# Optimization experiments

Hardware: AMD Instinct MI355X
Metric: run time of the kernel (lower is better)

## Reference

```python
import jax, jax.numpy as jnp
import numpy as np
import math

DIM = 1024
N_HEADS = 16
HEAD_DIM = DIM // N_HEADS


def setup_inputs() -> dict:
    key = jax.random.key(0)
    kx, kk, kq, kv = jax.random.split(key, 4)
    x = jax.random.normal(kx, (4, 2048, DIM), dtype=jnp.float32)
    # torch.rand -> uniform [0,1)
    wk = jax.random.uniform(kk, (N_HEADS, DIM, HEAD_DIM), dtype=jnp.float32)
    wq = jax.random.uniform(kq, (N_HEADS, DIM, HEAD_DIM), dtype=jnp.float32)
    wv = jax.random.uniform(kv, (N_HEADS, DIM, HEAD_DIM), dtype=jnp.float32)
    return {"x": x, "wk": wk, "wq": wq, "wv": wv}


def reference(x, wk, wq, wv):
    # x: [b, l, d]; w*: [n, d, e]
    k = jnp.einsum('bld,nde->bnle', x, wk)
    q = jnp.einsum('bld,nde->bnle', x, wq)
    v = jnp.einsum('bld,nde->bnle', x, wv)
    head_dim = k.shape[-1]
    scores = jnp.einsum('bnle,bnme->bnlm', q, k) / math.sqrt(head_dim)
    s = jax.nn.softmax(scores, axis=-1)
    r = jnp.einsum('bnlm,bnme->blne', s, v)  # [b, l, n, e]
    b, l, n, e = r.shape
    return r.reshape(b, l, n * e)
```

## Files before the change

kernel.cpp:

```cpp
#include <hip/hip_runtime.h>
#include <math.h>

#define DIMX   1024
#define NHEADS 16
#define HD     64
#define BATCH  4
#define SEQ    2048
#define NM     (BATCH * NHEADS * SEQ * HD)

typedef unsigned short ushort_t;
typedef __attribute__((ext_vector_type(8))) short bf16x8;
typedef __attribute__((ext_vector_type(4))) short bf16x4;
typedef __attribute__((ext_vector_type(4))) float f32x4;

#define MFMA16(a, b, c) __builtin_amdgcn_mfma_f32_16x16x32_bf16(a, b, c, 0, 0, 0)

#if __has_builtin(__builtin_amdgcn_mfma_f32_16x16x16bf16_1k)
#define MFMA_PV(a, b, c) __builtin_amdgcn_mfma_f32_16x16x16bf16_1k(a, b, c, 0, 0, 0)
#else
static __device__ __forceinline__ f32x4 mfma_pv_asm(bf16x4 a, bf16x4 b, f32x4 c) {
    asm("v_mfma_f32_16x16x16_bf16 %0, %1, %2, %0" : "+v"(c) : "v"(a), "v"(b));
    return c;
}
#define MFMA_PV(a, b, c) mfma_pv_asm(a, b, c)
#endif

__device__ __forceinline__ ushort_t f2bf(float x) {
    unsigned u = __float_as_uint(x);
    u += 0x7fffu + ((u >> 16) & 1u);
    return (ushort_t)(u >> 16);
}
__device__ __forceinline__ float bf2f(ushort_t h) {
    return __uint_as_float(((unsigned)h) << 16);
}

__device__ __forceinline__ unsigned pack_bf16_trunc(float lo, float hi) {
#if __has_builtin(__builtin_amdgcn_perm)
    return __builtin_amdgcn_perm(__float_as_uint(hi), __float_as_uint(lo), 0x07060302u);
#else
    return (__float_as_uint(lo) >> 16) | (__float_as_uint(hi) & 0xFFFF0000u);
#endif
}
__device__ __forceinline__ float trunc_bf(float x) {
    return __uint_as_float(__float_as_uint(x) & 0xFFFF0000u);
}

__device__ __forceinline__ float fast_exp2(float x) {
#if __has_builtin(__builtin_amdgcn_exp2f)
    return __builtin_amdgcn_exp2f(x);
#else
    return exp2f(x);
#endif
}

#define GLOAD_LDS16(g, l) \
    __builtin_amdgcn_global_load_lds((const __attribute__((address_space(1))) unsigned int*)(g), \
                                     (__attribute__((address_space(3))) unsigned int*)(l), 16, 0, 0)

__global__ __launch_bounds__(256) void convert_x(
    const float* __restrict__ x, ushort_t* __restrict__ Xh, ushort_t* __restrict__ Xl)
{
    int i = blockIdx.x * 256 + threadIdx.x;
    #pragma unroll
    for (int t = 0; t < 4; t++) {
        int idx = t * 524288 + i;
        f32x4 v = ((const f32x4*)x)[idx];
        ushort4 hi, lo;
        hi.x = f2bf(v[0]); lo.x = f2bf(v[0] - bf2f(hi.x));
        hi.y = f2bf(v[1]); lo.y = f2bf(v[1] - bf2f(hi.y));
        hi.z = f2bf(v[2]); lo.z = f2bf(v[2] - bf2f(hi.z));
        hi.w = f2bf(v[3]); lo.w = f2bf(v[3] - bf2f(hi.w));
        ((ushort4*)Xh)[idx] = hi;
        ((ushort4*)Xl)[idx] = lo;
    }
}

__global__ __launch_bounds__(256) void convert_w(
    const float* __restrict__ wk, const float* __restrict__ wq, const float* __restrict__ wv,
    ushort_t* __restrict__ Bqh, ushort_t* __restrict__ Bql, ushort_t* __restrict__ Bvh)
{
    __shared__ float Ts[64][65];
    const int bid = blockIdx.x;
    const int mat = bid >> 8;
    const int rem = bid & 255;
    const int n  = rem >> 4;
    const int dt = rem & 15;
    const float* w = (mat == 0) ? wq : (mat == 1) ? wk : wv;
    const int tid = threadIdx.x;

    #pragma unroll
    for (int t = 0; t < 16; t++) {
        int i = tid + t * 256;
        int r = i >> 6, e = i & 63;
        Ts[r][e] = w[((size_t)n * 1024 + dt * 64 + r) * 64 + e];
    }
    __syncthreads();
    #pragma unroll
    for (int t = 0; t < 16; t++) {
        int i = tid + t * 256;
        int e = i >> 6, r = i & 63;
        float v = Ts[r][e];
        ushort_t hi = f2bf(v);
        size_t o = (size_t)(n * 64 + e) * 1024 + dt * 64 + r;
        if (mat < 2) {
            Bqh[(size_t)mat * 1048576 + o] = hi;
            Bql[(size_t)mat * 1048576 + o] = f2bf(v - bf2f(hi));
        } else {
            Bvh[o] = hi;
        }
    }
}

__global__ __launch_bounds__(256) void proj_qk(
    const ushort_t* __restrict__ Xh, const ushort_t* __restrict__ Xl,
    const ushort_t* __restrict__ Bh, const ushort_t* __restrict__ Bl,
    float* __restrict__ Qf, ushort_t* __restrict__ Khi, ushort_t* __restrict__ Klo)
{
    __shared__ __align__(16) ushort_t Ah[128 * 64];
    __shared__ __align__(16) ushort_t Al[128 * 64];
    __shared__ __align__(16) ushort_t Bhs[128 * 64];
    __shared__ __align__(16) ushort_t Bls[128 * 64];

    const int mt = blockIdx.x, nt = blockIdx.y;
    const int tid = threadIdx.x;
    const int w = tid >> 6, lane = tid & 63, col = lane & 15, quad = lane >> 4;
    const int wm = w & 1, wn = w >> 1;

    f32x4 acc[4][4] = {};

    for (int kc = 0; kc < 1024; kc += 64) {
        __syncthreads();
        #pragma unroll
        for (int i = 0; i < 4; i++) {
            int s = (w * 4 + i) * 64 + lane;
            int r = s >> 3, j = s & 7, g = j ^ (r & 7);
            size_t aoff = (size_t)(mt * 128 + r) * 1024 + kc + g * 8;
            size_t boff = (size_t)(nt * 128 + r) * 1024 + kc + g * 8;
            GLOAD_LDS16(Xh + aoff, Ah  + (size_t)(w * 4 + i) * 512);
            GLOAD_LDS16(Xl + aoff, Al  + (size_t)(w * 4 + i) * 512);
            GLOAD_LDS16(Bh + boff, Bhs + (size_t)(w * 4 + i) * 512);
            GLOAD_LDS16(Bl + boff, Bls + (size_t)(w * 4 + i) * 512);
        }
        __syncthreads();
        #pragma unroll
        for (int kk = 0; kk < 2; kk++) {
            bf16x8 a_h[4], a_l[4], b_h[4], b_l[4];
            const int gi = kk * 4 + quad;
            #pragma unroll
            for (int t = 0; t < 4; t++) {
                int rA = wm * 64 + t * 16 + col;
                int jA = gi ^ (rA & 7);
                a_h[t] = *(const bf16x8*)&Ah[(rA * 8 + jA) * 8];
                a_l[t] = *(const bf16x8*)&Al[(rA * 8 + jA) * 8];
                int rB = wn * 64 + t * 16 + col;
                int jB = gi ^ (rB & 7);
                b_h[t] = *(const bf16x8*)&Bhs[(rB * 8 + jB) * 8];
                b_l[t] = *(const bf16x8*)&Bls[(rB * 8 + jB) * 8];
            }
            #pragma unroll
            for (int t = 0; t < 4; t++)
                #pragma unroll
                for (int u = 0; u < 4; u++) {
                    acc[t][u] = MFMA16(a_h[t], b_h[u], acc[t][u]);
                    acc[t][u] = MFMA16(a_l[t], b_h[u], acc[t][u]);
                    acc[t][u] = MFMA16(a_h[t], b_l[u], acc[t][u]);
                }
        }
    }

    const bool isQ = (nt < 8);
    #pragma unroll
    for (int t = 0; t < 4; t++) {
        #pragma unroll
        for (int u = 0; u < 4; u++) {
            int np = nt * 128 + wn * 64 + u * 16 + col;
            int head = (np >> 6) & 15, e = np & 63;
            #pragma unroll
            for (int rr = 0; rr < 4; rr++) {
                int mm = mt * 128 + wm * 64 + t * 16 + quad * 4 + rr;
                int bi = mm >> 11, l = mm & 2047;
                size_t base = (((size_t)bi * NHEADS + head) * SEQ + l) * HD + e;
                float v = acc[t][u][rr];
                if (isQ) {
                    Qf[base] = v;
                } else {
                    ushort_t hi = f2bf(v);
                    Khi[base] = hi;
                    Klo[base] = f2bf(v - bf2f(hi));
                }
            }
        }
    }
}

__global__ __launch_bounds__(256) void proj_v(
    const ushort_t* __restrict__ Wvh, const ushort_t* __restrict__ Xh,
    ushort_t* __restrict__ Vt)
{
    __shared__ __align__(16) ushort_t Ah[128 * 64];
    __shared__ __align__(16) ushort_t Bhs[128 * 64];

    const int mt = blockIdx.x, nt = blockIdx.y;
    const int tid = threadIdx.x;
    const int w = tid >> 6, lane = tid & 63, col = lane & 15, quad = lane >> 4;
    const int wm = w & 1, wn = w >> 1;

    f32x4 acc[4][4] = {};

    for (int kc = 0; kc < 1024; kc += 64) {
        __syncthreads();
        #pragma unroll
        for (int i = 0; i < 4; i++) {
            int s = (w * 4 + i) * 64 + lane;
            int r = s >> 3, j = s & 7, g = j ^ (r & 7);
            size_t aoff = (size_t)(mt * 128 + r) * 1024 + kc + g * 8;
            size_t boff = (size_t)(nt * 128 + r) * 1024 + kc + g * 8;
            GLOAD_LDS16(Wvh + aoff, Ah  + (size_t)(w * 4 + i) * 512);
            GLOAD_LDS16(Xh  + boff, Bhs + (size_t)(w * 4 + i) * 512);
        }
        __syncthreads();
        #pragma unroll
        for (int kk = 0; kk < 2; kk++) {
            bf16x8 a_h[4], b_h[4];
            const int gi = kk * 4 + quad;
            #pragma unroll
            for (int t = 0; t < 4; t++) {
                int rA = wm * 64 + t * 16 + col;
                a_h[t] = *(const bf16x8*)&Ah[(rA * 8 + (gi ^ (rA & 7))) * 8];
                int rB = wn * 64 + t * 16 + col;
                b_h[t] = *(const bf16x8*)&Bhs[(rB * 8 + (gi ^ (rB & 7))) * 8];
            }
            #pragma unroll
            for (int t = 0; t < 4; t++)
                #pragma unroll
                for (int u = 0; u < 4; u++)
                    acc[t][u] = MFMA16(a_h[t], b_h[u], acc[t][u]);
        }
    }

    #pragma unroll
    for (int t = 0; t < 4; t++) {
        #pragma unroll
        for (int rr = 0; rr < 4; rr++) {
            int ep = mt * 128 + wm * 64 + t * 16 + quad * 4 + rr;
            int head = ep >> 6, e = ep & 63;
            #pragma unroll
            for (int u = 0; u < 4; u++) {
                int lg = nt * 128 + wn * 64 + u * 16 + col;
                int bi = lg >> 11, l = lg & 2047;
                Vt[(((size_t)bi * NHEADS + head) * HD + e) * SEQ + l] = f2bf(acc[t][u][rr]);
            }
        }
    }
}

__global__ __launch_bounds__(256, 4) void attn_mfma_kernel(
    const float* __restrict__ Qf, const ushort_t* __restrict__ Khi,
    const ushort_t* __restrict__ Klo, const ushort_t* __restrict__ Vt,
    float* __restrict__ out)
{
    __shared__ __align__(16) ushort_t Khs0[64 * 64];
    __shared__ __align__(16) ushort_t Kls0[64 * 64];
    __shared__ __align__(16) ushort_t Vts0[64 * 64];
    __shared__ __align__(16) ushort_t Khs1[64 * 64];
    __shared__ __align__(16) ushort_t Kls1[64 * 64];
    __shared__ __align__(16) ushort_t Vts1[64 * 64];

    const int qt  = blockIdx.x;
    const int bn  = blockIdx.y;
    const int tid = threadIdx.x;
    const int w    = tid >> 6;
    const int lane = tid & 63;
    const int col  = lane & 15;
    const int quad = lane >> 4;

    const ushort_t* Kh_g = Khi + (size_t)bn * SEQ * HD;
    const ushort_t* Kl_g = Klo + (size_t)bn * SEQ * HD;
    const ushort_t* Vt_g = Vt  + (size_t)bn * HD * SEQ;

    union { bf16x8 v; short s[8]; } qh[2], ql[2];
    {
        const int qrow = qt * 64 + w * 16 + col;
        const float* qp = Qf + ((size_t)bn * SEQ + qrow) * HD;
        #pragma unroll
        for (int ks = 0; ks < 2; ks++) {
            float qv[8];
            f32x4 a = *(const f32x4*)(qp + ks * 32 + quad * 8);
            f32x4 b = *(const f32x4*)(qp + ks * 32 + quad * 8 + 4);
            qv[0]=a[0]; qv[1]=a[1]; qv[2]=a[2]; qv[3]=a[3];
            qv[4]=b[0]; qv[5]=b[1]; qv[6]=b[2]; qv[7]=b[3];
            #pragma unroll
            for (int j = 0; j < 8; j++) {
                float xsc = qv[j] * (0.125f * 1.44269504088896f);
                ushort_t hi = f2bf(xsc);
                ushort_t lo = f2bf(xsc - bf2f(hi));
                qh[ks].s[j] = (short)hi;
                ql[ks].s[j] = (short)lo;
            }
        }
    }

    f32x4 O[4] = {};
    float m_i = -1e30f;
    float L   = 0.f;

#define STAGE(CH, KHD, KLD, VTD) do {                                         \
    _Pragma("unroll")                                                         \
    for (int t_ = 0; t_ < 2; t_++) {                                          \
        int G_   = (w * 2 + t_) * 64 + lane;                                  \
        int key_ = G_ >> 3;                                                   \
        int blk_ = (G_ & 7) ^ (key_ & 7);                                     \
        size_t koff_ = (size_t)((CH) * 64 + key_) * HD + blk_ * 8;            \
        size_t voff_ = (size_t)key_ * SEQ + (CH) * 64 + blk_ * 8;             \
        GLOAD_LDS16(Kh_g + koff_, (KHD) + (w * 2 + t_) * 512);                \
        GLOAD_LDS16(Kl_g + koff_, (KLD) + (w * 2 + t_) * 512);                \
        GLOAD_LDS16(Vt_g + voff_, (VTD) + (w * 2 + t_) * 512);                \
    }                                                                         \
} while (0)

#define CHUNK_COMPUTE(KHS, KLS, VTS) do {                                     \
    f32x4 St[4] = {};                                                         \
    _Pragma("unroll")                                                         \
    for (int ks = 0; ks < 2; ks++) {                                          \
        _Pragma("unroll")                                                     \
        for (int t = 0; t < 4; t++) {                                         \
            int key = t * 16 + col;                                           \
            int g = key * 8 + ((ks * 4 + quad) ^ (key & 7));                  \
            bf16x8 kh = *(const bf16x8*)&(KHS)[g * 8];                        \
            bf16x8 kl = *(const bf16x8*)&(KLS)[g * 8];                        \
            St[t] = MFMA16(kh, qh[ks].v, St[t]);                              \
            St[t] = MFMA16(kh, ql[ks].v, St[t]);                              \
            St[t] = MFMA16(kl, qh[ks].v, St[t]);                              \
        }                                                                     \
    }                                                                         \
    float mx = St[0][0];                                                      \
    _Pragma("unroll")                                                         \
    for (int t = 0; t < 4; t++)                                               \
        _Pragma("unroll")                                                     \
        for (int r = 0; r < 4; r++) mx = fmaxf(mx, St[t][r]);                 \
    mx = fmaxf(mx, __shfl_xor(mx, 16));                                       \
    mx = fmaxf(mx, __shfl_xor(mx, 32));                                       \
    if (__any(mx > m_i - 30.0f)) {                                            \
        float mnew = fmaxf(m_i, mx);                                          \
        float al   = fast_exp2(m_i - mnew);                                   \
        m_i = mnew;                                                           \
        bf16x4 vfrag[4][4];                                                   \
        _Pragma("unroll")                                                     \
        for (int u = 0; u < 4; u++) {                                         \
            int rowbase = (u * 16 + col) * 64;                                \
            _Pragma("unroll")                                                 \
            for (int t = 0; t < 4; t++) {                                     \
                int g = (t * 2 + (quad >> 1)) ^ (col & 7);                    \
                vfrag[u][t] = *(const bf16x4*)&(VTS)[rowbase + g * 8 + (quad & 1) * 4]; \
            }                                                                 \
        }                                                                     \
        float psum = 0.f;                                                     \
        bf16x4 pf[4];                                                         \
        _Pragma("unroll")                                                     \
        for (int t = 0; t < 4; t++) {                                         \
            float p0 = fast_exp2(St[t][0] - mnew);                            \
            float p1 = fast_exp2(St[t][1] - mnew);                            \
            float p2 = fast_exp2(St[t][2] - mnew);                            \
            float p3 = fast_exp2(St[t][3] - mnew);                            \
            psum += trunc_bf(p0) + trunc_bf(p1) + trunc_bf(p2) + trunc_bf(p3);\
            union { unsigned u[2]; bf16x4 v; } pk;                            \
            pk.u[0] = pack_bf16_trunc(p0, p1);                                \
            pk.u[1] = pack_bf16_trunc(p2, p3);                                \
            pf[t] = pk.v;                                                     \
        }                                                                     \
        L = L * al + psum;                                                    \
        _Pragma("unroll")                                                     \
        for (int u = 0; u < 4; u++) {                                         \
            O[u][0] *= al; O[u][1] *= al;                                     \
            O[u][2] *= al; O[u][3] *= al;                                     \
        }                                                                     \
        _Pragma("unroll")                                                     \
        for (int t = 0; t < 4; t++)                                           \
            _Pragma("unroll")                                                 \
            for (int u = 0; u < 4; u++)                                       \
                O[u] = MFMA_PV(vfrag[u][t], pf[t], O[u]);                     \
    }                                                                         \
} while (0)

    STAGE(0, Khs0, Kls0, Vts0);
    __syncthreads();

    for (int ch = 0; ch < 30; ch += 2) {
        STAGE(ch + 1, Khs1, Kls1, Vts1);
        CHUNK_COMPUTE(Khs0, Kls0, Vts0);
        __syncthreads();
        STAGE(ch + 2, Khs0, Kls0, Vts0);
        CHUNK_COMPUTE(Khs1, Kls1, Vts1);
        __syncthreads();
    }
    STAGE(31, Khs1, Kls1, Vts1);
    CHUNK_COMPUTE(Khs0, Kls0, Vts0);
    __syncthreads();
    CHUNK_COMPUTE(Khs1, Kls1, Vts1);

#undef STAGE
#undef CHUNK_COMPUTE

    const int b = bn >> 4, n = bn & 15;
    {
        float Lr = L;
        Lr += __shfl_xor(Lr, 16);
        Lr += __shfl_xor(Lr, 32);
        float inv = 1.0f / Lr;
        int l = qt * 64 + w * 16 + col;
        size_t base = ((size_t)(b * SEQ + l)) * (NHEADS * HD) + n * HD;
        #pragma unroll
        for (int u = 0; u < 4; u++) {
            f32x4 o;
            o[0] = O[u][0] * inv; o[1] = O[u][1] * inv;
            o[2] = O[u][2] * inv; o[3] = O[u][3] * inv;
            *(f32x4*)&out[base + u * 16 + quad * 4] = o;
        }
    }
}

extern "C" void kernel_launch(void* const* d_in, const int* in_sizes, int n_in,
                              void* d_out, int out_size, void* d_ws, size_t ws_size,
                              hipStream_t stream) {
    const float* x  = (const float*)d_in[0];
    const float* wk = (const float*)d_in[1];
    const float* wq = (const float*)d_in[2];
    const float* wv = (const float*)d_in[3];
    float* out = (float*)d_out;

    ushort_t* Xh  = (ushort_t*)d_ws;
    ushort_t* Xl  = Xh + NM;
    ushort_t* Vt  = Xl;
    ushort_t* Bqh = Xl + NM;
    ushort_t* Bql = Bqh + 2097152;
    ushort_t* Bvh = Bql + 2097152;
    float*    Qf  = (float*)(Bvh + 1048576);
    ushort_t* Khi = (ushort_t*)(Qf + NM);
    ushort_t* Klo = Khi + NM;

    convert_x<<<2048, 256, 0, stream>>>(x, Xh, Xl);
    convert_w<<<768, 256, 0, stream>>>(wk, wq, wv, Bqh, Bql, Bvh);
    proj_qk<<<dim3(64, 16), 256, 0, stream>>>(Xh, Xl, Bqh, Bql, Qf, Khi, Klo);
    proj_v<<<dim3(8, 64), 256, 0, stream>>>(Bvh, Xh, Vt);
    attn_mfma_kernel<<<dim3(32, 64), 256, 0, stream>>>(Qf, Khi, Klo, Vt, out);
}
```

Baseline: 369.6 us.

## Use 512-thread attention blocks, XCD-aware block mapping, and lazy hi/lo score correction

Each attention block now has 8 waves covering 128 query rows, so one K/V chunk staged in LDS serves twice as many queries, and each thread issues a single staging load per buffer. Blocks are remapped so that the same (batch, head) lands on the same XCD, which should improve L2 reuse of K and V. QK^T first runs a cheap hi*hi MFMA pass, and only when a chunk could contribute (threshold widened to 46) does it add the hi*lo and lo*hi correction terms. This cuts MFMA work for chunks that are skipped, but it adds a duplicate LDS read pass and a second max reduction, and the skip decision now rests on the less precise scores.

```diff
diff --git a/kernel.cpp b/kernel.cpp
--- a/kernel.cpp
+++ b/kernel.cpp
@@ -254,7 +254,7 @@
     }
 }
 
-__global__ __launch_bounds__(256, 4) void attn_mfma_kernel(
+__global__ __launch_bounds__(512, 4) void attn_mfma_kernel(
     const float* __restrict__ Qf, const ushort_t* __restrict__ Khi,
     const ushort_t* __restrict__ Klo, const ushort_t* __restrict__ Vt,
     float* __restrict__ out)
@@ -266,8 +266,11 @@
     __shared__ __align__(16) ushort_t Kls1[64 * 64];
     __shared__ __align__(16) ushort_t Vts1[64 * 64];
 
-    const int qt  = blockIdx.x;
-    const int bn  = blockIdx.y;
+    const int linear = blockIdx.y * 16 + blockIdx.x;
+    const int xcd = linear & 7;
+    const int kk_ = linear >> 3;
+    const int bn  = xcd + 8 * (kk_ >> 4);
+    const int qt  = kk_ & 15;
     const int tid = threadIdx.x;
     const int w    = tid >> 6;
     const int lane = tid & 63;
@@ -280,7 +283,7 @@
 
     union { bf16x8 v; short s[8]; } qh[2], ql[2];
     {
-        const int qrow = qt * 64 + w * 16 + col;
+        const int qrow = qt * 128 + w * 16 + col;
         const float* qp = Qf + ((size_t)bn * SEQ + qrow) * HD;
         #pragma unroll
         for (int ks = 0; ks < 2; ks++) {
@@ -305,17 +308,14 @@
     float L   = 0.f;
 
 #define STAGE(CH, KHD, KLD, VTD) do {                                         \
-    _Pragma("unroll")                                                         \
-    for (int t_ = 0; t_ < 2; t_++) {                                          \
-        int G_   = (w * 2 + t_) * 64 + lane;                                  \
-        int key_ = G_ >> 3;                                                   \
-        int blk_ = (G_ & 7) ^ (key_ & 7);                                     \
-        size_t koff_ = (size_t)((CH) * 64 + key_) * HD + blk_ * 8;            \
-        size_t voff_ = (size_t)key_ * SEQ + (CH) * 64 + blk_ * 8;             \
-        GLOAD_LDS16(Kh_g + koff_, (KHD) + (w * 2 + t_) * 512);                \
-        GLOAD_LDS16(Kl_g + koff_, (KLD) + (w * 2 + t_) * 512);                \
-        GLOAD_LDS16(Vt_g + voff_, (VTD) + (w * 2 + t_) * 512);                \
-    }                                                                         \
+    int G_   = tid;                                                           \
+    int key_ = G_ >> 3;                                                       \
+    int blk_ = (G_ & 7) ^ (key_ & 7);                                         \
+    size_t koff_ = (size_t)((CH) * 64 + key_) * HD + blk_ * 8;                \
+    size_t voff_ = (size_t)key_ * SEQ + (CH) * 64 + blk_ * 8;                 \
+    GLOAD_LDS16(Kh_g + koff_, (KHD) + w * 512);                               \
+    GLOAD_LDS16(Kl_g + koff_, (KLD) + w * 512);                               \
+    GLOAD_LDS16(Vt_g + voff_, (VTD) + w * 512);                               \
 } while (0)
 
 #define CHUNK_COMPUTE(KHS, KLS, VTS) do {                                     \
@@ -327,10 +327,7 @@
             int key = t * 16 + col;                                           \
             int g = key * 8 + ((ks * 4 + quad) ^ (key & 7));                  \
             bf16x8 kh = *(const bf16x8*)&(KHS)[g * 8];                        \
-            bf16x8 kl = *(const bf16x8*)&(KLS)[g * 8];                        \
             St[t] = MFMA16(kh, qh[ks].v, St[t]);                              \
-            St[t] = MFMA16(kh, ql[ks].v, St[t]);                              \
-            St[t] = MFMA16(kl, qh[ks].v, St[t]);                              \
         }                                                                     \
     }                                                                         \
     float mx = St[0][0];                                                      \
@@ -340,8 +337,27 @@
         for (int r = 0; r < 4; r++) mx = fmaxf(mx, St[t][r]);                 \
     mx = fmaxf(mx, __shfl_xor(mx, 16));                                       \
     mx = fmaxf(mx, __shfl_xor(mx, 32));                                       \
-    if (__any(mx > m_i - 30.0f)) {                                            \
-        float mnew = fmaxf(m_i, mx);                                          \
+    if (__any(mx > m_i - 46.0f)) {                                            \
+        _Pragma("unroll")                                                     \
+        for (int ks = 0; ks < 2; ks++) {                                      \
+            _Pragma("unroll")                                                 \
+            for (int t = 0; t < 4; t++) {                                     \
+                int key = t * 16 + col;                                       \
+                int g = key * 8 + ((ks * 4 + quad) ^ (key & 7));              \
+                bf16x8 kh = *(const bf16x8*)&(KHS)[g * 8];                    \
+                bf16x8 kl = *(const bf16x8*)&(KLS)[g * 8];                    \
+                St[t] = MFMA16(kh, ql[ks].v, St[t]);                          \
+                St[t] = MFMA16(kl, qh[ks].v, St[t]);                          \
+            }                                                                 \
+        }                                                                     \
+        float mxe = St[0][0];                                                 \
+        _Pragma("unroll")                                                     \
+        for (int t = 0; t < 4; t++)                                           \
+            _Pragma("unroll")                                                 \
+            for (int r = 0; r < 4; r++) mxe = fmaxf(mxe, St[t][r]);           \
+        mxe = fmaxf(mxe, __shfl_xor(mxe, 16));                                \
+        mxe = fmaxf(mxe, __shfl_xor(mxe, 32));                                \
+        float mnew = fmaxf(m_i, mxe);                                         \
         float al   = fast_exp2(m_i - mnew);                                   \
         m_i = mnew;                                                           \
         bf16x4 vfrag[4][4];                                                   \
@@ -407,7 +423,7 @@
         Lr += __shfl_xor(Lr, 16);
         Lr += __shfl_xor(Lr, 32);
         float inv = 1.0f / Lr;
-        int l = qt * 64 + w * 16 + col;
+        int l = qt * 128 + w * 16 + col;
         size_t base = ((size_t)(b * SEQ + l)) * (NHEADS * HD) + n * HD;
         #pragma unroll
         for (int u = 0; u < 4; u++) {
@@ -442,5 +458,5 @@
     convert_w<<<768, 256, 0, stream>>>(wk, wq, wv, Bqh, Bql, Bvh);
     proj_qk<<<dim3(64, 16), 256, 0, stream>>>(Xh, Xl, Bqh, Bql, Qf, Khi, Klo);
     proj_v<<<dim3(8, 64), 256, 0, stream>>>(Bvh, Xh, Vt);
-    attn_mfma_kernel<<<dim3(32, 64), 256, 0, stream>>>(Qf, Khi, Klo, Vt, out);
-}
+    attn_mfma_kernel<<<dim3(16, 64), 512, 0, stream>>>(Qf, Khi, Klo, Vt, out);
+}
```

Measured after the change: 339.1 us. 1.09x faster.
